# Kernel optimization log

Hardware: AMD Instinct MI355X
Metric: run time of the kernel (lower is better)

Reference implementation:

```python
import jax, jax.numpy as jnp
from jax import lax
import numpy as np

B, T, D, H, W = 256, 1024, 4, 64, 128

# Tsit5 Butcher tableau
C2, C3, C4, C5 = 0.161, 0.327, 0.9, 0.9800255409045097
A21 = 0.161
A31, A32 = -0.008480655492356989, 0.335480655492357
A41, A42, A43 = 2.8971530571054935, -6.359448489975075, 4.3622954328695815
A51, A52, A53, A54 = 5.325864828439257, -11.748883564062828, 7.4955393428898365, -0.09249506636175525
A61, A62, A63, A64, A65 = 5.86145544294642, -12.92096931784711, 8.159367898576159, -0.071584973281401, -0.028269050394068383
BW1, BW2, BW3, BW4, BW5, BW6 = 0.09646076681806523, 0.01, 0.4798896504144996, 1.379008574103742, -3.290069515436081, 2.324710524099774


def setup_inputs() -> dict:
    key = jax.random.key(0)
    ks = jax.random.split(key, 20)
    f32 = jnp.float32
    ts = jnp.arange(T, dtype=f32)
    coef = lambda k: 0.1 * jax.random.normal(k, (B, T - 1, D), f32)
    g = lambda k, shp, fan: jax.random.normal(k, shp, f32) / np.sqrt(fan)
    return {
        'ts': ts,
        'coef_d': coef(ks[0]), 'coef_c': coef(ks[1]),
        'coef_b': coef(ks[2]), 'coef_a': coef(ks[3]),
        # initial MLP: D -> W -> W -> H (softplus hidden, identity final)
        'W0': g(ks[4], (W, D), D), 'b0': jnp.zeros((W,), f32),
        'W1': g(ks[5], (W, W), W), 'b1': jnp.zeros((W,), f32),
        'W2': g(ks[6], (H, W), W), 'b2': jnp.zeros((H,), f32),
        # vector-field MLP: H -> W -> W -> H*D (softplus hidden, tanh final)
        'F0': g(ks[7], (W, H), H), 'g0': jnp.zeros((W,), f32),
        'F1': g(ks[8], (W, W), W), 'g1': jnp.zeros((W,), f32),
        'F2': g(ks[9], (H * D, W), W), 'g2': jnp.zeros((H * D,), f32),
        # readout: H -> 3
        'L': g(ks[10], (3, H), H), 'lb': jnp.zeros((3,), f32),
        'evolving_out': 1,
    }


def reference(ts, coef_d, coef_c, coef_b, coef_a,
              W0, b0, W1, b1, W2, b2,
              F0, g0, F1, g1, F2, g2, L, lb, evolving_out):
    sp = jax.nn.softplus

    def vf(y, dx):  # y: (B,H), dx: (B,D) -> f(y) @ dX/dt : (B,H)
        h1 = sp(y @ F0.T + g0)
        h2 = sp(h1 @ F1.T + g1)
        f = jnp.tanh(h2 @ F2.T + g2).reshape(-1, H, D)
        return jnp.einsum('bhd,bd->bh', f, dx)

    def step(y, inp):
        dt, cb, cc, cd = inp  # dt scalar; cb/cc/cd: (B,D) cubic coeffs of interval
        dx = lambda frac: cb + frac * (2.0 * cc + 3.0 * frac * cd)
        k1 = vf(y, dx(0.0))
        k2 = vf(y + dt * (A21 * k1), dx(C2 * dt))
        k3 = vf(y + dt * (A31 * k1 + A32 * k2), dx(C3 * dt))
        k4 = vf(y + dt * (A41 * k1 + A42 * k2 + A43 * k3), dx(C4 * dt))
        k5 = vf(y + dt * (A51 * k1 + A52 * k2 + A53 * k3 + A54 * k4), dx(C5 * dt))
        k6 = vf(y + dt * (A61 * k1 + A62 * k2 + A63 * k3 + A64 * k4 + A65 * k5), dx(dt))
        ynew = y + dt * (BW1 * k1 + BW2 * k2 + BW3 * k3 + BW4 * k4 + BW5 * k5 + BW6 * k6)
        return ynew, ynew

    # y0 = initial_mlp(X(t0)); X(t0) = coef_a at first interval (frac = 0)
    x0 = coef_a[:, 0]  # (B,D)
    h1 = sp(x0 @ W0.T + b0)
    h2 = sp(h1 @ W1.T + b1)
    y0 = h2 @ W2.T + b2  # (B,H)

    dts = ts[1:] - ts[:-1]  # (T-1,)
    xs = (dts, coef_b.transpose(1, 0, 2), coef_c.transpose(1, 0, 2), coef_d.transpose(1, 0, 2))
    ylast, ys = lax.scan(step, y0, xs)  # ys: (T-1,B,H)

    if evolving_out:
        ys_all = jnp.concatenate([y0[None], ys], axis=0)  # (T,B,H)
        return jnp.einsum('tbh,oh->bto', ys_all, L) + lb  # (B,T,3)
    return ylast @ L.T + lb  # (B,3)
```

## Files before the change

### kernel.cpp

```cpp
#include <hip/hip_runtime.h>

namespace {

constexpr int NB    = 256;
constexpr int NT    = 1024;
constexpr int NSTEP = NT - 1;
constexpr int D = 4, H = 64, W = 128;

constexpr float cAT[6][5] = {
    {0.f, 0.f, 0.f, 0.f, 0.f},
    {0.161f, 0.f, 0.f, 0.f, 0.f},
    {-0.008480655492356989f, 0.335480655492357f, 0.f, 0.f, 0.f},
    {2.8971530571054935f, -6.359448489975075f, 4.3622954328695815f, 0.f, 0.f},
    {5.325864828439257f, -11.748883564062828f, 7.4955393428898365f, -0.09249506636175525f, 0.f},
    {5.86145544294642f, -12.92096931784711f, 8.159367898576159f, -0.071584973281401f, -0.028269050394068383f}};
constexpr float cFR[6] = {0.0f, 0.161f, 0.327f, 0.9f, 0.9800255409045097f, 1.0f};
constexpr float cBW[6] = {0.09646076681806523f, 0.01f, 0.4798896504144996f,
                          1.379008574103742f, -3.290069515436081f, 2.324710524099774f};

__device__ __forceinline__ float softplus_f(float x) {
    float e = __expf(-fabsf(x));
    return fmaxf(x, 0.0f) + __logf(1.0f + e);
}
__device__ __forceinline__ float tanh_f(float x) {
    float e = __expf(2.0f * x);
    return 1.0f - __fdividef(2.0f, 1.0f + e);
}

template <int CTRL>
__device__ __forceinline__ float dppmv(float x) {
    return __int_as_float(__builtin_amdgcn_mov_dpp(__float_as_int(x), CTRL, 0xF, 0xF, true));
}

__device__ __forceinline__ int pY(int i)  { return (i >> 4) * 20 + (i & 15); }
__device__ __forceinline__ int p1i(int i) { return (i >> 5) * 36 + (i & 31); }
__device__ __forceinline__ int p2i(int i) { return (i >> 6) * 72 + (i & 63); }

__global__ __launch_bounds__(512, 2)
void cde_kernel(const float* __restrict__ ts,
                const float* __restrict__ coef_d,
                const float* __restrict__ coef_c,
                const float* __restrict__ coef_b,
                const float* __restrict__ coef_a,
                const float* __restrict__ W0, const float* __restrict__ b0,
                const float* __restrict__ W1, const float* __restrict__ b1,
                const float* __restrict__ W2, const float* __restrict__ b2,
                const float* __restrict__ F0, const float* __restrict__ g0,
                const float* __restrict__ F1, const float* __restrict__ g1,
                const float* __restrict__ F2, const float* __restrict__ g2,
                const float* __restrict__ Lm, const float* __restrict__ lb,
                float* __restrict__ out)
{
    const int b    = blockIdx.x;
    const int tid  = threadIdx.x;

    const int j12  = tid >> 2;
    const int q12  = tid & 3;
    const int og   = tid >> 3;
    const int q2   = tid & 7;
    const int grp  = tid >> 2;
    const int qc   = tid & 3;
    const int g3   = tid >> 3;
    const int dsel = ((tid >> 2) & 1) * 2 + (tid & 1);

    __shared__ __align__(16) float s_ys[80];
    __shared__ __align__(16) float s_h1[144];
    __shared__ __align__(16) float s_h2[136];

    float wA[16];
    float wB0[16], wB1[16];
    float wC0[32], wC1[32];
    #pragma unroll
    for (int i = 0; i < 16; i += 4) {
        float4 v = *reinterpret_cast<const float4*>(F0 + j12 * H + q12 * 16 + i);
        wA[i+0]=v.x; wA[i+1]=v.y; wA[i+2]=v.z; wA[i+3]=v.w;
    }
    #pragma unroll
    for (int i = 0; i < 16; i += 4) {
        float4 v0 = *reinterpret_cast<const float4*>(F1 + (2*og)     * W + q2 * 16 + i);
        float4 v1 = *reinterpret_cast<const float4*>(F1 + (2*og + 1) * W + q2 * 16 + i);
        wB0[i+0]=v0.x; wB0[i+1]=v0.y; wB0[i+2]=v0.z; wB0[i+3]=v0.w;
        wB1[i+0]=v1.x; wB1[i+1]=v1.y; wB1[i+2]=v1.z; wB1[i+3]=v1.w;
    }
    #pragma unroll
    for (int i = 0; i < 32; i += 4) {
        float4 v0 = *reinterpret_cast<const float4*>(F2 + (2*grp)     * W + qc * 32 + i);
        float4 v1 = *reinterpret_cast<const float4*>(F2 + (2*grp + 1) * W + qc * 32 + i);
        wC0[i+0]=v0.x; wC0[i+1]=v0.y; wC0[i+2]=v0.z; wC0[i+3]=v0.w;
        wC1[i+0]=v1.x; wC1[i+1]=v1.y; wC1[i+2]=v1.z; wC1[i+3]=v1.w;
    }
    const float g0r = g0[j12];
    const float g1s = g1[2*og  + (q2  & 1)];
    const float g2s = g2[2*grp + (tid & 1)];
    const float L0r = Lm[0*H + (tid & 63)];
    const float L1r = Lm[1*H + (tid & 63)];
    const float L2r = Lm[2*H + (tid & 63)];
    const float lb0 = lb[0], lb1 = lb[1], lb2 = lb[2];

    const float* pA = s_ys + q12 * 20;
    const float* pB = s_h1 + (q2 >> 1) * 36 + (q2 & 1) * 16;
    const float* pC = s_h2 + (qc >> 1) * 72 + (qc & 1) * 32;
    float* pw1 = s_h1 + p1i(j12);
    float* pw2 = s_h2 + p2i(2*og + (q2 & 1));
    float* pwy = s_ys + pY(g3);

    if (tid < W) {
        const float4 x0 = *reinterpret_cast<const float4*>(coef_a + (size_t)b * NSTEP * D);
        const float4 w  = *reinterpret_cast<const float4*>(W0 + tid * D);
        s_h1[p1i(tid)] = softplus_f(w.x*x0.x + w.y*x0.y + w.z*x0.z + w.w*x0.w + b0[tid]);
    }
    __syncthreads();
    if (tid < W) {
        float a = b1[tid];
        #pragma unroll
        for (int blk = 0; blk < 4; ++blk)
            #pragma unroll
            for (int i = 0; i < 8; ++i) {
                float4 wv = *reinterpret_cast<const float4*>(W1 + tid * W + blk * 32 + 4 * i);
                float4 hv = *reinterpret_cast<const float4*>(s_h1 + blk * 36 + 4 * i);
                a += wv.x*hv.x + wv.y*hv.y + wv.z*hv.z + wv.w*hv.w;
            }
        s_h2[p2i(tid)] = softplus_f(a);
    }
    __syncthreads();
    if (tid < H) {
        float a = b2[tid];
        #pragma unroll
        for (int blk = 0; blk < 2; ++blk)
            #pragma unroll
            for (int i = 0; i < 16; ++i) {
                float4 wv = *reinterpret_cast<const float4*>(W2 + tid * W + blk * 64 + 4 * i);
                float4 hv = *reinterpret_cast<const float4*>(s_h2 + blk * 72 + 4 * i);
                a += wv.x*hv.x + wv.y*hv.y + wv.z*hv.z + wv.w*hv.w;
            }
        s_ys[pY(tid)] = a;
    }
    __syncthreads();

    float y = s_ys[pY(g3)];

    auto project = [&](int tslot) {
        if (tid < 64) {
            float yv = s_ys[pY(tid)];
            float p0 = yv * L0r, p1 = yv * L1r, p2 = yv * L2r;
            #pragma unroll
            for (int off = 32; off >= 1; off >>= 1) {
                p0 += __shfl_xor(p0, off);
                p1 += __shfl_xor(p1, off);
                p2 += __shfl_xor(p2, off);
            }
            if (tid == 0) {
                float* dst = out + ((size_t)b * NT + tslot) * 3;
                dst[0] = p0 + lb0; dst[1] = p1 + lb1; dst[2] = p2 + lb2;
            }
        }
    };
    project(0);

    const float* cb_pl = coef_b + (size_t)b * NSTEP * D + dsel;
    const float* cc_pl = coef_c + (size_t)b * NSTEP * D + dsel;
    const float* cd_pl = coef_d + (size_t)b * NSTEP * D + dsel;

    for (int t = 0; t < NSTEP; ++t) {
        const float cbd = cb_pl[(size_t)t * D];
        const float ccd = cc_pl[(size_t)t * D];
        const float cdd = cd_pl[(size_t)t * D];
        const float dtv = ts[t + 1] - ts[t];

        float k[6];

        #pragma unroll
        for (int s = 0; s < 6; ++s) {
            {
                float4 h0 = *reinterpret_cast<const float4*>(pA + 0);
                float4 h1 = *reinterpret_cast<const float4*>(pA + 4);
                float4 h2 = *reinterpret_cast<const float4*>(pA + 8);
                float4 h3 = *reinterpret_cast<const float4*>(pA + 12);
                float a1  = wA[0]*h0.x + wA[1]*h0.y + wA[2]*h0.z + wA[3]*h0.w
                          + wA[4]*h1.x + wA[5]*h1.y + wA[6]*h1.z + wA[7]*h1.w;
                float a1b = wA[8]*h2.x + wA[9]*h2.y + wA[10]*h2.z + wA[11]*h2.w
                          + wA[12]*h3.x + wA[13]*h3.y + wA[14]*h3.z + wA[15]*h3.w;
                float a1s = a1 + a1b;
                a1s += dppmv<0xB1>(a1s);
                a1s += dppmv<0x4E>(a1s);
                if (q12 == 0) *pw1 = softplus_f(a1s + g0r);
            }
            __syncthreads();

            {
                float4 u0 = *reinterpret_cast<const float4*>(pB + 0);
                float4 u1 = *reinterpret_cast<const float4*>(pB + 4);
                float4 u2 = *reinterpret_cast<const float4*>(pB + 8);
                float4 u3 = *reinterpret_cast<const float4*>(pB + 12);
                float p0 = wB0[0]*u0.x + wB0[1]*u0.y + wB0[2]*u0.z + wB0[3]*u0.w
                         + wB0[4]*u1.x + wB0[5]*u1.y + wB0[6]*u1.z + wB0[7]*u1.w
                         + wB0[8]*u2.x + wB0[9]*u2.y + wB0[10]*u2.z + wB0[11]*u2.w
                         + wB0[12]*u3.x + wB0[13]*u3.y + wB0[14]*u3.z + wB0[15]*u3.w;
                float p1 = wB1[0]*u0.x + wB1[1]*u0.y + wB1[2]*u0.z + wB1[3]*u0.w
                         + wB1[4]*u1.x + wB1[5]*u1.y + wB1[6]*u1.z + wB1[7]*u1.w
                         + wB1[8]*u2.x + wB1[9]*u2.y + wB1[10]*u2.z + wB1[11]*u2.w
                         + wB1[12]*u3.x + wB1[13]*u3.y + wB1[14]*u3.z + wB1[15]*u3.w;
                p0 += dppmv<0xB1>(p0); p1 += dppmv<0xB1>(p1);
                p0 += dppmv<0x4E>(p0); p1 += dppmv<0x4E>(p1);
                p0 += dppmv<0x141>(p0); p1 += dppmv<0x141>(p1);
                float spv = softplus_f(((q2 & 1) ? p1 : p0) + g1s);
                if (q2 < 2) *pw2 = spv;
            }
            __syncthreads();

            {
                float p0 = 0.f, p1 = 0.f;
                #pragma unroll
                for (int m = 0; m < 8; ++m) {
                    float4 u = *reinterpret_cast<const float4*>(pC + 4*m);
                    p0 += wC0[4*m+0]*u.x + wC0[4*m+1]*u.y + wC0[4*m+2]*u.z + wC0[4*m+3]*u.w;
                    p1 += wC1[4*m+0]*u.x + wC1[4*m+1]*u.y + wC1[4*m+2]*u.z + wC1[4*m+3]*u.w;
                }
                p0 += dppmv<0xB1>(p0); p1 += dppmv<0xB1>(p1);
                p0 += dppmv<0x4E>(p0); p1 += dppmv<0x4E>(p1);
                const float ft = tanh_f(((tid & 1) ? p1 : p0) + g2s);

                const float frac = cFR[s] * dtv;
                const float dxd  = fmaf(frac, fmaf(3.0f * frac, cdd, 2.0f * ccd), cbd);
                float pk = ft * dxd * 0.5f;
                pk += dppmv<0xB1>(pk);
                pk += dppmv<0x4E>(pk);
                pk += dppmv<0x141>(pk);
                k[s] = pk;

                float ysn;
                if (s < 5) {
                    float acc = 0.f;
                    #pragma unroll
                    for (int i = 0; i <= s; ++i) acc = fmaf(cAT[s+1][i], k[i], acc);
                    ysn = fmaf(dtv, acc, y);
                } else {
                    float acc = 0.f;
                    #pragma unroll
                    for (int i = 0; i < 6; ++i) acc = fmaf(cBW[i], k[i], acc);
                    ysn = fmaf(dtv, acc, y);
                }
                if ((tid & 7) == 0) *pwy = ysn;
            }
            __syncthreads();
        }

        y = *pwy;
        project(t + 1);
    }
}

}

extern "C" void kernel_launch(void* const* d_in, const int* in_sizes, int n_in,
                              void* d_out, int out_size, void* d_ws, size_t ws_size,
                              hipStream_t stream) {
    const float* ts     = (const float*)d_in[0];
    const float* coef_d = (const float*)d_in[1];
    const float* coef_c = (const float*)d_in[2];
    const float* coef_b = (const float*)d_in[3];
    const float* coef_a = (const float*)d_in[4];
    const float* W0 = (const float*)d_in[5];
    const float* b0 = (const float*)d_in[6];
    const float* W1 = (const float*)d_in[7];
    const float* b1 = (const float*)d_in[8];
    const float* W2 = (const float*)d_in[9];
    const float* b2 = (const float*)d_in[10];
    const float* F0 = (const float*)d_in[11];
    const float* g0 = (const float*)d_in[12];
    const float* F1 = (const float*)d_in[13];
    const float* g1 = (const float*)d_in[14];
    const float* F2 = (const float*)d_in[15];
    const float* g2 = (const float*)d_in[16];
    const float* Lm = (const float*)d_in[17];
    const float* lb = (const float*)d_in[18];
    float* out = (float*)d_out;

    hipLaunchKernelGGL(cde_kernel, dim3(NB), dim3(512), 0, stream,
                       ts, coef_d, coef_c, coef_b, coef_a,
                       W0, b0, W1, b1, W2, b2,
                       F0, g0, F1, g1, F2, g2, Lm, lb, out);
}
```

Before: 6.208 ms.

## Double threads per block to 1024 and halve per-thread dot-product work

Blocks grow from 512 to 1024 threads, and all three MLP layers are split across twice as many lanes with half the weights held in registers per thread. The reductions are rebuilt around a 16-lane DPP pattern with a paired-output exchange, and the dX contraction rescaling changes from 0.5 to 0.25. This shortens each thread's serial FMA chain on the latency-bound sequential time loop. In exchange it adds cross-lane reduction steps and more waves taking part in each barrier, and the larger block and changed launch bounds may alter occupancy.

```diff
diff --git a/kernel.cpp b/kernel.cpp
--- a/kernel.cpp
+++ b/kernel.cpp
@@ -36,7 +36,7 @@
 __device__ __forceinline__ int p1i(int i) { return (i >> 5) * 36 + (i & 31); }
 __device__ __forceinline__ int p2i(int i) { return (i >> 6) * 72 + (i & 63); }
 
-__global__ __launch_bounds__(512, 2)
+__global__ __launch_bounds__(1024, 4)
 void cde_kernel(const float* __restrict__ ts,
                 const float* __restrict__ coef_d,
                 const float* __restrict__ coef_c,
@@ -54,55 +54,64 @@
     const int b    = blockIdx.x;
     const int tid  = threadIdx.x;
 
-    const int j12  = tid >> 2;
-    const int q12  = tid & 3;
-    const int og   = tid >> 3;
-    const int q2   = tid & 7;
-    const int grp  = tid >> 2;
-    const int qc   = tid & 3;
-    const int g3   = tid >> 3;
-    const int dsel = ((tid >> 2) & 1) * 2 + (tid & 1);
+    const int par  = tid & 1;
+    const int qAB  = tid & 15;
+    const int pg   = tid >> 4;
+    const int qc   = tid & 7;
+    const int cg   = tid >> 3;
+    const int dsel = ((tid >> 3) & 1) * 2 + par;
 
     __shared__ __align__(16) float s_ys[80];
     __shared__ __align__(16) float s_h1[144];
     __shared__ __align__(16) float s_h2[136];
 
-    float wA[16];
-    float wB0[16], wB1[16];
-    float wC0[32], wC1[32];
+    float wA0[4], wA1[4];
+    float wB0[8], wB1[8];
+    float wC0[16], wC1[16];
+    {
+        float4 v0 = *reinterpret_cast<const float4*>(F0 + (2*pg)     * H + 4*qAB);
+        float4 v1 = *reinterpret_cast<const float4*>(F0 + (2*pg + 1) * H + 4*qAB);
+        wA0[0]=v0.x; wA0[1]=v0.y; wA0[2]=v0.z; wA0[3]=v0.w;
+        wA1[0]=v1.x; wA1[1]=v1.y; wA1[2]=v1.z; wA1[3]=v1.w;
+    }
+    #pragma unroll
+    for (int i = 0; i < 8; i += 4) {
+        float4 v0 = *reinterpret_cast<const float4*>(F1 + (2*pg)     * W + 8*qAB + i);
+        float4 v1 = *reinterpret_cast<const float4*>(F1 + (2*pg + 1) * W + 8*qAB + i);
+        wB0[i+0]=v0.x; wB0[i+1]=v0.y; wB0[i+2]=v0.z; wB0[i+3]=v0.w;
+        wB1[i+0]=v1.x; wB1[i+1]=v1.y; wB1[i+2]=v1.z; wB1[i+3]=v1.w;
+    }
     #pragma unroll
     for (int i = 0; i < 16; i += 4) {
-        float4 v = *reinterpret_cast<const float4*>(F0 + j12 * H + q12 * 16 + i);
-        wA[i+0]=v.x; wA[i+1]=v.y; wA[i+2]=v.z; wA[i+3]=v.w;
-    }
-    #pragma unroll
-    for (int i = 0; i < 16; i += 4) {
-        float4 v0 = *reinterpret_cast<const float4*>(F1 + (2*og)     * W + q2 * 16 + i);
-        float4 v1 = *reinterpret_cast<const float4*>(F1 + (2*og + 1) * W + q2 * 16 + i);
-        wB0[i+0]=v0.x; wB0[i+1]=v0.y; wB0[i+2]=v0.z; wB0[i+3]=v0.w;
-        wB1[i+0]=v1.x; wB1[i+1]=v1.y; wB1[i+2]=v1.z; wB1[i+3]=v1.w;
-    }
-    #pragma unroll
-    for (int i = 0; i < 32; i += 4) {
-        float4 v0 = *reinterpret_cast<const float4*>(F2 + (2*grp)     * W + qc * 32 + i);
-        float4 v1 = *reinterpret_cast<const float4*>(F2 + (2*grp + 1) * W + qc * 32 + i);
+        float4 v0 = *reinterpret_cast<const float4*>(F2 + (2*cg)     * W + 16*qc + i);
+        float4 v1 = *reinterpret_cast<const float4*>(F2 + (2*cg + 1) * W + 16*qc + i);
         wC0[i+0]=v0.x; wC0[i+1]=v0.y; wC0[i+2]=v0.z; wC0[i+3]=v0.w;
         wC1[i+0]=v1.x; wC1[i+1]=v1.y; wC1[i+2]=v1.z; wC1[i+3]=v1.w;
     }
-    const float g0r = g0[j12];
-    const float g1s = g1[2*og  + (q2  & 1)];
-    const float g2s = g2[2*grp + (tid & 1)];
+    const float g0s = g0[2*pg + par];
+    const float g1s = g1[2*pg + par];
+    const float g2s = g2[2*cg + par];
     const float L0r = Lm[0*H + (tid & 63)];
     const float L1r = Lm[1*H + (tid & 63)];
     const float L2r = Lm[2*H + (tid & 63)];
     const float lb0 = lb[0], lb1 = lb[1], lb2 = lb[2];
 
-    const float* pA = s_ys + q12 * 20;
-    const float* pB = s_h1 + (q2 >> 1) * 36 + (q2 & 1) * 16;
-    const float* pC = s_h2 + (qc >> 1) * 72 + (qc & 1) * 32;
-    float* pw1 = s_h1 + p1i(j12);
-    float* pw2 = s_h2 + p2i(2*og + (q2 & 1));
-    float* pwy = s_ys + pY(g3);
+    const float* pA = s_ys + (qAB >> 2) * 20 + (qAB & 3) * 4;
+    const float* pB = s_h1 + (qAB >> 2) * 36 + (qAB & 3) * 8;
+    const float* pC = s_h2 + (qc  >> 2) * 72 + (qc  & 3) * 16;
+    float* pw1 = s_h1 + p1i(2*pg + par);
+    float* pw2 = s_h2 + p2i(2*pg + par);
+    float* pwy = s_ys + pY(pg);
+
+    auto red16 = [&](float p0, float p1) -> float {
+        float s = par ? p1 : p0;
+        float o = par ? p0 : p1;
+        s += dppmv<0xB1>(o);
+        s += dppmv<0x4E>(s);
+        s += dppmv<0x128>(s);
+        s += dppmv<0x124>(s);
+        return s;
+    };
 
     if (tid < W) {
         const float4 x0 = *reinterpret_cast<const float4*>(coef_a + (size_t)b * NSTEP * D);
@@ -137,7 +146,7 @@
     }
     __syncthreads();
 
-    float y = s_ys[pY(g3)];
+    float y = s_ys[pY(pg)];
 
     auto project = [&](int tslot) {
         if (tid < 64) {
@@ -172,60 +181,46 @@
         #pragma unroll
         for (int s = 0; s < 6; ++s) {
             {
-                float4 h0 = *reinterpret_cast<const float4*>(pA + 0);
-                float4 h1 = *reinterpret_cast<const float4*>(pA + 4);
-                float4 h2 = *reinterpret_cast<const float4*>(pA + 8);
-                float4 h3 = *reinterpret_cast<const float4*>(pA + 12);
-                float a1  = wA[0]*h0.x + wA[1]*h0.y + wA[2]*h0.z + wA[3]*h0.w
-                          + wA[4]*h1.x + wA[5]*h1.y + wA[6]*h1.z + wA[7]*h1.w;
-                float a1b = wA[8]*h2.x + wA[9]*h2.y + wA[10]*h2.z + wA[11]*h2.w
-                          + wA[12]*h3.x + wA[13]*h3.y + wA[14]*h3.z + wA[15]*h3.w;
-                float a1s = a1 + a1b;
-                a1s += dppmv<0xB1>(a1s);
-                a1s += dppmv<0x4E>(a1s);
-                if (q12 == 0) *pw1 = softplus_f(a1s + g0r);
+                float4 hv = *reinterpret_cast<const float4*>(pA);
+                float p0 = wA0[0]*hv.x + wA0[1]*hv.y + wA0[2]*hv.z + wA0[3]*hv.w;
+                float p1 = wA1[0]*hv.x + wA1[1]*hv.y + wA1[2]*hv.z + wA1[3]*hv.w;
+                float c = red16(p0, p1);
+                if (qAB < 2) *pw1 = softplus_f(c + g0s);
             }
             __syncthreads();
 
             {
                 float4 u0 = *reinterpret_cast<const float4*>(pB + 0);
                 float4 u1 = *reinterpret_cast<const float4*>(pB + 4);
-                float4 u2 = *reinterpret_cast<const float4*>(pB + 8);
-                float4 u3 = *reinterpret_cast<const float4*>(pB + 12);
                 float p0 = wB0[0]*u0.x + wB0[1]*u0.y + wB0[2]*u0.z + wB0[3]*u0.w
-                         + wB0[4]*u1.x + wB0[5]*u1.y + wB0[6]*u1.z + wB0[7]*u1.w
-                         + wB0[8]*u2.x + wB0[9]*u2.y + wB0[10]*u2.z + wB0[11]*u2.w
-                         + wB0[12]*u3.x + wB0[13]*u3.y + wB0[14]*u3.z + wB0[15]*u3.w;
+                         + wB0[4]*u1.x + wB0[5]*u1.y + wB0[6]*u1.z + wB0[7]*u1.w;
                 float p1 = wB1[0]*u0.x + wB1[1]*u0.y + wB1[2]*u0.z + wB1[3]*u0.w
-                         + wB1[4]*u1.x + wB1[5]*u1.y + wB1[6]*u1.z + wB1[7]*u1.w
-                         + wB1[8]*u2.x + wB1[9]*u2.y + wB1[10]*u2.z + wB1[11]*u2.w
-                         + wB1[12]*u3.x + wB1[13]*u3.y + wB1[14]*u3.z + wB1[15]*u3.w;
-                p0 += dppmv<0xB1>(p0); p1 += dppmv<0xB1>(p1);
-                p0 += dppmv<0x4E>(p0); p1 += dppmv<0x4E>(p1);
-                p0 += dppmv<0x141>(p0); p1 += dppmv<0x141>(p1);
-                float spv = softplus_f(((q2 & 1) ? p1 : p0) + g1s);
-                if (q2 < 2) *pw2 = spv;
+                         + wB1[4]*u1.x + wB1[5]*u1.y + wB1[6]*u1.z + wB1[7]*u1.w;
+                float c = red16(p0, p1);
+                if (qAB < 2) *pw2 = softplus_f(c + g1s);
             }
             __syncthreads();
 
             {
                 float p0 = 0.f, p1 = 0.f;
                 #pragma unroll
-                for (int m = 0; m < 8; ++m) {
+                for (int m = 0; m < 4; ++m) {
                     float4 u = *reinterpret_cast<const float4*>(pC + 4*m);
                     p0 += wC0[4*m+0]*u.x + wC0[4*m+1]*u.y + wC0[4*m+2]*u.z + wC0[4*m+3]*u.w;
                     p1 += wC1[4*m+0]*u.x + wC1[4*m+1]*u.y + wC1[4*m+2]*u.z + wC1[4*m+3]*u.w;
                 }
                 p0 += dppmv<0xB1>(p0); p1 += dppmv<0xB1>(p1);
                 p0 += dppmv<0x4E>(p0); p1 += dppmv<0x4E>(p1);
-                const float ft = tanh_f(((tid & 1) ? p1 : p0) + g2s);
+                p0 += dppmv<0x141>(p0); p1 += dppmv<0x141>(p1);
+                const float ft = tanh_f((par ? p1 : p0) + g2s);
 
                 const float frac = cFR[s] * dtv;
                 const float dxd  = fmaf(frac, fmaf(3.0f * frac, cdd, 2.0f * ccd), cbd);
-                float pk = ft * dxd * 0.5f;
+                float pk = ft * dxd * 0.25f;
                 pk += dppmv<0xB1>(pk);
                 pk += dppmv<0x4E>(pk);
-                pk += dppmv<0x141>(pk);
+                pk += dppmv<0x128>(pk);
+                pk += dppmv<0x124>(pk);
                 k[s] = pk;
 
                 float ysn;
@@ -240,7 +235,7 @@
                     for (int i = 0; i < 6; ++i) acc = fmaf(cBW[i], k[i], acc);
                     ysn = fmaf(dtv, acc, y);
                 }
-                if ((tid & 7) == 0) *pwy = ysn;
+                if ((tid & 15) == 0) *pwy = ysn;
             }
             __syncthreads();
         }
@@ -276,7 +271,7 @@
     const float* lb = (const float*)d_in[18];
     float* out = (float*)d_out;
 
-    hipLaunchKernelGGL(cde_kernel, dim3(NB), dim3(512), 0, stream,
+    hipLaunchKernelGGL(cde_kernel, dim3(NB), dim3(1024), 0, stream,
                        ts, coef_d, coef_c, coef_b, coef_a,
                        W0, b0, W1, b1, W2, b2,
                        F0, g0, F1, g1, F2, g2, Lm, lb, out);
```

Measured after the change: 7.102 ms. 14.4% more time.
